# Kernel tuning notes

Measured on AMD Instinct MI355X. Metric: run time of the kernel, lower is better.

## Reference

```python
import jax, jax.numpy as jnp
import numpy as np
import math

HIDDEN = 1024

def setup_inputs() -> dict:
    key = jax.random.key(0)
    k1, k2, k3, k4, k5 = jax.random.split(key, 5)
    s = 1.0 / math.sqrt(HIDDEN)
    return {
        "x": jax.random.normal(k1, (4, 2048, HIDDEN), dtype=jnp.float32),
        "W_qkv": jax.random.uniform(k2, (HIDDEN, 3 * HIDDEN), jnp.float32, -s, s),
        "b_qkv": jax.random.uniform(k3, (3 * HIDDEN,), jnp.float32, -s, s),
        "W_out": jax.random.uniform(k4, (HIDDEN, HIDDEN), jnp.float32, -s, s),
        "b_out": jax.random.uniform(k5, (HIDDEN,), jnp.float32, -s, s),
    }

def reference(x, W_qkv, b_qkv, W_out, b_out):
    # fused QKV projection: [b, s, 3h]
    qkv = jnp.einsum("bsh,hd->bsd", x, W_qkv) + b_qkv
    q, k, v = jnp.split(qkv, 3, axis=-1)
    scale = 1.0 / math.sqrt(x.shape[-1])
    scores = jnp.einsum("bqh,bkh->bqk", q, k) * scale  # [b, s, s]
    attn = jax.nn.softmax(scores, axis=-1)
    out = jnp.einsum("bqk,bkh->bqh", attn, v)
    return jnp.einsum("bsh,hd->bsd", out, W_out) + b_out
```

## Files before the change

kernel.cpp:

```cpp
#include <hip/hip_runtime.h>
#include <cstdint>
#include <cstddef>


typedef __bf16 bf16;
typedef __bf16 bf16x8 __attribute__((ext_vector_type(8)));
typedef __bf16 bf16x4 __attribute__((ext_vector_type(4)));
typedef float  f32x4  __attribute__((ext_vector_type(4)));

#define UNIT 8192

__device__ __forceinline__ void gload_lds16(const bf16* g, bf16* l) {
  __builtin_amdgcn_global_load_lds(
      (const __attribute__((address_space(1))) unsigned int*)g,
      (__attribute__((address_space(3))) unsigned int*)l, 16, 0, 0);
}

#define GATE(N)  asm volatile("s_waitcnt vmcnt(" #N ")" ::: "memory")
#define LGKM0()  asm volatile("s_waitcnt lgkmcnt(0)" ::: "memory")
#define SBAR()   __builtin_amdgcn_s_barrier()
#define SCHED0() __builtin_amdgcn_sched_barrier(0)

#define BK97 32
#define U97  4096

__device__ __forceinline__ void stage97(const bf16* g0, long ld, bf16* u, int tid) {
  const int wv = tid >> 6;
  #pragma unroll
  for (int j = 0; j < 2; ++j) {
    const int c = j * 256 + tid;
    const int r = c >> 2, s = c & 3;
    const int sg = s ^ ((r >> 1) & 3);
    const int cb = j * 256 + (wv << 6);
    gload_lds16(g0 + (long)r * ld + sg * 8, u + (size_t)cb * 8);
  }
}

__device__ __forceinline__ bf16x8 rd97(const bf16* u, int r, int s) {
  return *(const bf16x8*)(u + (size_t)r * 32 + (size_t)((s ^ ((r >> 1) & 3)) * 8));
}

template <int MODE>
__device__ __forceinline__ void gemm97_body(
    const bf16* __restrict__ A, long sAz, int lda,
    const bf16* __restrict__ B, long sBz, int ldb, int K,
    bf16* __restrict__ p0, long sCz, int ldc,
    bf16* __restrict__ p1, bf16* __restrict__ p2,
    float* __restrict__ fout, long sFz,
    const float* __restrict__ bias, float scale) {
  __shared__ bf16 lds[3][2][U97];
  const int tid = threadIdx.x;
  const int wv = tid >> 6, ln = tid & 63;
  const int wr = wv >> 1, wc = wv & 1;
  const int lr = ln & 15, lh = ln >> 4;
  const int m0 = blockIdx.x * 128, n0 = blockIdx.y * 128;
  const int z = blockIdx.z;
  const bf16* Ag = A + (long)z * sAz + (long)m0 * lda;
  const bf16* Bg = B + (long)z * sBz + (long)n0 * ldb;
  const int NT = K / BK97;

  stage97(Ag,        lda, &lds[0][0][0], tid);
  stage97(Bg,        ldb, &lds[0][1][0], tid);
  stage97(Ag + BK97, lda, &lds[1][0][0], tid);
  stage97(Bg + BK97, ldb, &lds[1][1][0], tid);
  GATE(4);
  SCHED0();
  SBAR();

  f32x4 acc[4][4];
  #pragma unroll
  for (int i = 0; i < 4; ++i)
    #pragma unroll
    for (int j = 0; j < 4; ++j) acc[i][j] = f32x4{0.f, 0.f, 0.f, 0.f};

  int rs = 0, ns = 2;
  for (int t = 0; t < NT; ++t) {
    const bf16* Au = &lds[rs][0][0];
    const bf16* Bu = &lds[rs][1][0];
    const bool pf = (t + 2 < NT);
    bf16x8 aF[4], bF[4];
    #pragma unroll
    for (int i = 0; i < 4; ++i) aF[i] = rd97(Au, wr * 64 + i * 16 + lr, lh);
    #pragma unroll
    for (int j = 0; j < 4; ++j) bF[j] = rd97(Bu, wc * 64 + j * 16 + lr, lh);
    if (pf) {
      stage97(Ag + (long)(t + 2) * BK97, lda, &lds[ns][0][0], tid);
      stage97(Bg + (long)(t + 2) * BK97, ldb, &lds[ns][1][0], tid);
    }
    LGKM0();
    SCHED0();
    __builtin_amdgcn_s_setprio(1);
    #pragma unroll
    for (int i = 0; i < 4; ++i)
      #pragma unroll
      for (int j = 0; j < 4; ++j)
        acc[i][j] = __builtin_amdgcn_mfma_f32_16x16x32_bf16(aF[i], bF[j], acc[i][j], 0, 0, 0);
    __builtin_amdgcn_s_setprio(0);
    if (t + 1 < NT) {
      if (pf) { GATE(4); } else { GATE(0); }
      SCHED0();
      SBAR();
    }
    rs = (rs == 2) ? 0 : rs + 1;
    ns = (ns == 2) ? 0 : ns + 1;
  }

  #pragma unroll
  for (int mf = 0; mf < 4; ++mf) {
    #pragma unroll
    for (int nf = 0; nf < 4; ++nf) {
      #pragma unroll
      for (int rg = 0; rg < 4; ++rg) {
        const int gm = m0 + wr * 64 + mf * 16 + lh * 4 + rg;
        const int gn = n0 + wc * 64 + nf * 16 + lr;
        float v = acc[mf][nf][rg];
        if constexpr (MODE == 0) {
          v += bias[gn];
          if (gn < 1024)       p0[(size_t)gm * 1024 + gn] = (bf16)v;
          else if (gn < 2048)  p1[(size_t)gm * 1024 + (gn - 1024)] = (bf16)v;
          else                 p2[(size_t)gm * 1024 + (gn - 2048)] = (bf16)v;
        } else if constexpr (MODE == 2) {
          p0[(size_t)z * sCz + (size_t)gm * ldc + gn] = (bf16)(v * scale);
        } else {
          fout[(size_t)z * sFz + (size_t)gm * ldc + gn] = v + bias[gn];
        }
      }
    }
  }
}

#define GEMM_ARGS const bf16* A, long sAz, int lda, const bf16* B, long sBz, int ldb, \
                  int K, bf16* p0, long sCz, int ldc, bf16* p1, bf16* p2,             \
                  float* fout, long sFz, const float* bias, float scale
__global__ __launch_bounds__(256, 3) void gemm_qkv(GEMM_ARGS) {
  gemm97_body<0>(A, sAz, lda, B, sBz, ldb, K, p0, sCz, ldc, p1, p2, fout, sFz, bias, scale);
}
__global__ __launch_bounds__(256, 3) void gemm_vwt(GEMM_ARGS) {
  gemm97_body<2>(A, sAz, lda, B, sBz, ldb, K, p0, sCz, ldc, p1, p2, fout, sFz, bias, scale);
}
__global__ __launch_bounds__(256, 3) void gemm_pvw(GEMM_ARGS) {
  gemm97_body<3>(A, sAz, lda, B, sBz, ldb, K, p0, sCz, ldc, p1, p2, fout, sFz, bias, scale);
}

#define THREADS8 512

__device__ __forceinline__ void stage_unit(const bf16* g0, long ld, bf16* ldsu, int tid) {
  const int wv = tid >> 6;
  #pragma unroll
  for (int j = 0; j < 2; ++j) {
    const int c = j * 512 + tid;
    const int r = c >> 3;
    const int sg = (c & 7) ^ (r & 7);
    const int cb = j * 512 + (wv << 6);
    gload_lds16(g0 + (long)r * ld + sg * 8, ldsu + (size_t)cb * 8);
  }
}

__device__ __forceinline__ bf16x8 rd_frag(const bf16* unitb, int r, int s) {
  return *(const bf16x8*)(unitb + (size_t)r * 64 + (size_t)((s ^ (r & 7)) * 8));
}

#define PHASE(DB, MH, NH, RA, RB, STAGE_CODE, GATE_CODE)                         \
  {                                                                              \
    if (RA) {                                                                    \
      _Pragma("unroll") for (int mf = 0; mf < 4; ++mf)                           \
        _Pragma("unroll") for (int ks = 0; ks < 2; ++ks)                         \
          aF[mf][ks] = rd_frag(&lds[DB][MH][0], wsm * 64 + mf * 16 + lr, ks * 4 + lh); \
    }                                                                            \
    if (RB) {                                                                    \
      _Pragma("unroll") for (int nf = 0; nf < 2; ++nf)                           \
        _Pragma("unroll") for (int ks = 0; ks < 2; ++ks)                         \
          bF[NH][nf][ks] = rd_frag(&lds[DB][2 + NH][0], wsn * 32 + nf * 16 + lr, ks * 4 + lh); \
    }                                                                            \
    STAGE_CODE;                                                                  \
    SBAR();                                                                      \
    LGKM0();                                                                     \
    SCHED0();                                                                    \
    __builtin_amdgcn_s_setprio(1);                                               \
    _Pragma("unroll") for (int mf = 0; mf < 4; ++mf)                             \
      _Pragma("unroll") for (int nf = 0; nf < 2; ++nf)                           \
        _Pragma("unroll") for (int ks = 0; ks < 2; ++ks)                         \
          acc[(MH)*4 + mf][(NH)*2 + nf] = __builtin_amdgcn_mfma_f32_16x16x32_bf16( \
              aF[mf][ks], bF[NH][nf][ks], acc[(MH)*4 + mf][(NH)*2 + nf], 0, 0, 0); \
    __builtin_amdgcn_s_setprio(0);                                               \
    GATE_CODE;                                                                   \
    SBAR();                                                                      \
    SCHED0();                                                                    \
  }

__global__ __launch_bounds__(THREADS8, 2) void gemm_sc(
    const bf16* __restrict__ A, long sAz, int lda,
    const bf16* __restrict__ B, long sBz, int ldb, int K,
    bf16* __restrict__ p0, long sCz, float scale) {
  __shared__ bf16 lds[2][4][UNIT];
  const int tid = threadIdx.x;
  const int wv = tid >> 6, ln = tid & 63;
  const int wsm = wv >> 2, wsn = wv & 3;
  const int lr = ln & 15, lh = ln >> 4;

  const int gx = gridDim.x, gy = gridDim.y;
  const int lin = blockIdx.x + gx * (blockIdx.y + gy * blockIdx.z);
  const int nwg = gx * gy * gridDim.z;
  const int swz = (lin & 7) * (nwg >> 3) + (lin >> 3);
  const int by = swz % gy;
  const int t2 = swz / gy;
  const int bx = t2 % gx;
  const int z  = t2 / gx;

  const int m0 = bx * 256, n0 = by * 256;
  const bf16* Ag = A + (long)z * sAz + (long)m0 * lda;
  const bf16* Bg = B + (long)z * sBz + (long)n0 * ldb;
  const int NITER = K / 128;

  stage_unit(Ag,             lda, &lds[0][0][0], tid);
  stage_unit(Bg,             ldb, &lds[0][2][0], tid);
  stage_unit(Ag + 128 * lda, lda, &lds[0][1][0], tid);
  stage_unit(Bg + 128 * ldb, ldb, &lds[0][3][0], tid);
  stage_unit(Ag + 64,        lda, &lds[1][0][0], tid);
  stage_unit(Bg + 64,        ldb, &lds[1][2][0], tid);
  GATE(8);
  SBAR();
  SCHED0();

  f32x4 acc[8][4];
  #pragma unroll
  for (int i = 0; i < 8; ++i)
    #pragma unroll
    for (int j = 0; j < 4; ++j) acc[i][j] = f32x4{0.f, 0.f, 0.f, 0.f};
  bf16x8 aF[4][2], bF[2][2][2];

  for (int it = 0; it < NITER; ++it) {
    const bool nl = (it + 1 < NITER);
    const long ktA = 2L * it + 1, ktB = 2L * it + 2, ktC = 2L * it + 3;
    PHASE(0, 0, 0, 1, 1,
      { stage_unit(Ag + 128 * lda + ktA * 64, lda, &lds[1][1][0], tid); },
      { GATE(6); });
    PHASE(0, 0, 1, 0, 1,
      { stage_unit(Bg + 128 * ldb + ktA * 64, ldb, &lds[1][3][0], tid); },
      { GATE(10); });
    PHASE(0, 1, 0, 1, 0,
      { if (nl) stage_unit(Ag + ktB * 64, lda, &lds[0][0][0], tid); },
      {});
    PHASE(0, 1, 1, 0, 0,
      { if (nl) stage_unit(Bg + ktB * 64, ldb, &lds[0][2][0], tid); },
      { if (nl) { GATE(8); } else { GATE(4); } });
    PHASE(1, 0, 0, 1, 1,
      { if (nl) stage_unit(Ag + 128 * lda + ktB * 64, lda, &lds[0][1][0], tid); },
      { if (nl) { GATE(6); } else { GATE(0); } });
    PHASE(1, 0, 1, 0, 1,
      { if (nl) stage_unit(Bg + 128 * ldb + ktB * 64, ldb, &lds[0][3][0], tid); },
      { GATE(10); });
    PHASE(1, 1, 0, 1, 0,
      { if (nl) stage_unit(Ag + ktC * 64, lda, &lds[1][0][0], tid); },
      {});
    PHASE(1, 1, 1, 0, 0,
      { if (nl) stage_unit(Bg + ktC * 64, ldb, &lds[1][2][0], tid); },
      { GATE(8); });
  }

  #pragma unroll
  for (int mi = 0; mi < 8; ++mi) {
    #pragma unroll
    for (int ni = 0; ni < 4; ++ni) {
      #pragma unroll
      for (int rg = 0; rg < 4; ++rg) {
        const int gm = m0 + (mi >> 2) * 128 + wsm * 64 + (mi & 3) * 16 + lh * 4 + rg;
        const int gn = n0 + (ni >> 1) * 128 + wsn * 32 + (ni & 1) * 16 + lr;
        p0[(size_t)z * sCz + (size_t)gm * 2048 + gn] = (bf16)(acc[mi][ni][rg] * scale);
      }
    }
  }
}

__global__ __launch_bounds__(256) void k_f32_to_bf16(const float* __restrict__ in,
                                                     bf16* __restrict__ out, long n) {
  long i = ((long)blockIdx.x * blockDim.x + threadIdx.x) * 4;
  if (i + 3 < n) {
    float4 v = *(const float4*)(in + i);
    bf16x4 o;
    o[0] = (bf16)v.x; o[1] = (bf16)v.y; o[2] = (bf16)v.z; o[3] = (bf16)v.w;
    *(bf16x4*)(out + i) = o;
  }
}

__global__ __launch_bounds__(256) void k_transpose(const float* __restrict__ in,
                                                   bf16* __restrict__ out, int R, int C) {
  __shared__ float t[32][33];
  int c0 = blockIdx.x * 32, r0 = blockIdx.y * 32;
  int tx = threadIdx.x, ty = threadIdx.y;
  #pragma unroll
  for (int dy = 0; dy < 32; dy += 8)
    t[ty + dy][tx] = in[(size_t)(r0 + ty + dy) * C + c0 + tx];
  __syncthreads();
  #pragma unroll
  for (int dy = 0; dy < 32; dy += 8)
    out[(size_t)(c0 + ty + dy) * R + r0 + tx] = (bf16)t[tx][ty + dy];
}

__global__ __launch_bounds__(256) void k_softmax(bf16* __restrict__ S) {
  const int row = blockIdx.x;
  bf16* p = S + (size_t)row * 2048;
  const int tid = threadIdx.x;
  bf16x8 vin = *(const bf16x8*)(p + tid * 8);
  float x[8];
  float mx = -1e30f;
  #pragma unroll
  for (int i = 0; i < 8; ++i) { x[i] = (float)vin[i]; mx = fmaxf(mx, x[i]); }
  #pragma unroll
  for (int off = 32; off; off >>= 1) mx = fmaxf(mx, __shfl_down(mx, off));
  __shared__ float redm[4];
  if ((tid & 63) == 0) redm[tid >> 6] = mx;
  __syncthreads();
  mx = fmaxf(fmaxf(redm[0], redm[1]), fmaxf(redm[2], redm[3]));
  float s = 0.f;
  #pragma unroll
  for (int i = 0; i < 8; ++i) { x[i] = __expf(x[i] - mx); s += x[i]; }
  #pragma unroll
  for (int off = 32; off; off >>= 1) s += __shfl_down(s, off);
  __shared__ float reds[4];
  if ((tid & 63) == 0) reds[tid >> 6] = s;
  __syncthreads();
  s = reds[0] + reds[1] + reds[2] + reds[3];
  float inv = 1.0f / s;
  bf16x8 vo;
  #pragma unroll
  for (int i = 0; i < 8; ++i) vo[i] = (bf16)(x[i] * inv);
  *(bf16x8*)(p + tid * 8) = vo;
}

extern "C" void kernel_launch(void* const* d_in, const int* in_sizes, int n_in,
                              void* d_out, int out_size, void* d_ws, size_t ws_size,
                              hipStream_t stream) {
  const float* x    = (const float*)d_in[0];
  const float* Wqkv = (const float*)d_in[1];
  const float* bqkv = (const float*)d_in[2];
  const float* Wout = (const float*)d_in[3];
  const float* bout = (const float*)d_in[4];
  float* out = (float*)d_out;

  char* w = (char*)d_ws;
  const size_t MB = 1ull << 20;
  bf16* Xb  = (bf16*)(w);
  bf16* WqT = (bf16*)(w + 16 * MB);
  bf16* WoT = (bf16*)(w + 22 * MB);
  bf16* Qb  = (bf16*)(w + 24 * MB);
  bf16* Kb  = (bf16*)(w + 40 * MB);
  bf16* Vb  = (bf16*)(w + 56 * MB);
  bf16* Sb  = (bf16*)(w + 72 * MB);
  bf16* VWT = (bf16*)(w + 104 * MB);

  k_f32_to_bf16<<<8192, 256, 0, stream>>>(x, Xb, 8388608L);
  dim3 tb(32, 8);
  k_transpose<<<dim3(96, 32), tb, 0, stream>>>(Wqkv, WqT, 1024, 3072);
  k_transpose<<<dim3(32, 32), tb, 0, stream>>>(Wout, WoT, 1024, 1024);

  gemm_qkv<<<dim3(64, 24), 256, 0, stream>>>(
      Xb, 0L, 1024, WqT, 0L, 1024, 1024,
      Qb, 0L, 1024, Kb, Vb, nullptr, 0L, bqkv, 1.0f);

  gemm_vwt<<<dim3(8, 16, 4), 256, 0, stream>>>(
      WoT, 0L, 1024, Vb, 2048L * 1024, 1024, 1024,
      VWT, 1024L * 2048, 2048, nullptr, nullptr, nullptr, 0L, nullptr, 1.0f);

  gemm_sc<<<dim3(8, 8, 4), THREADS8, 0, stream>>>(
      Qb, 2048L * 1024, 1024, Kb, 2048L * 1024, 1024, 1024,
      Sb, 2048L * 2048, 0.03125f);

  k_softmax<<<8192, 256, 0, stream>>>(Sb);

  gemm_pvw<<<dim3(16, 8, 4), 256, 0, stream>>>(
      Sb, 2048L * 2048, 2048, VWT, 1024L * 2048, 2048, 2048,
      nullptr, 0L, 1024, nullptr, nullptr, out, 2048L * 1024, bout, 1.0f);
}
```

Before: 209.9 us.

## Load B fragments directly from global into registers, bypassing LDS staging

The GEMM body no longer stages the B tile through LDS. Each wave loads its own B fragments from global memory straight into registers, double-buffered one k-step ahead, while A keeps its triple-buffered LDS pipeline. The loop is manually unrolled by two to alternate the register buffers. This halves LDS traffic and shared-memory footprint, but the B loads are now uncoalesced row-strided per-lane accesses that are repeated across the two wave rows, and their latency is exposed with only one step of prefetch.

```diff
diff --git a/kernel.cpp b/kernel.cpp
--- a/kernel.cpp
+++ b/kernel.cpp
@@ -9,6 +9,7 @@
 typedef float  f32x4  __attribute__((ext_vector_type(4)));
 
 #define UNIT 8192
+#define U97  4096
 
 __device__ __forceinline__ void gload_lds16(const bf16* g, bf16* l) {
   __builtin_amdgcn_global_load_lds(
@@ -20,9 +21,6 @@
 #define LGKM0()  asm volatile("s_waitcnt lgkmcnt(0)" ::: "memory")
 #define SBAR()   __builtin_amdgcn_s_barrier()
 #define SCHED0() __builtin_amdgcn_sched_barrier(0)
-
-#define BK97 32
-#define U97  4096
 
 __device__ __forceinline__ void stage97(const bf16* g0, long ld, bf16* u, int tid) {
   const int wv = tid >> 6;
@@ -38,6 +36,33 @@
 
 __device__ __forceinline__ bf16x8 rd97(const bf16* u, int r, int s) {
   return *(const bf16x8*)(u + (size_t)r * 32 + (size_t)((s ^ ((r >> 1) & 3)) * 8));
+}
+
+template <bool PF2, bool PF1>
+__device__ __forceinline__ void iter97(
+    int t, int rs, int ns, const bf16* Ag, long lda, const bf16* Bl, long ldb,
+    bf16 (*lds)[U97], bf16x8 (&bcur)[4], bf16x8 (&bnxt)[4],
+    f32x4 (&acc)[4][4], int tid, int wr, int lr, int lh) {
+  bf16x8 aF[4];
+  #pragma unroll
+  for (int i = 0; i < 4; ++i) aF[i] = rd97(&lds[rs][0], wr * 64 + i * 16 + lr, lh);
+  if (PF1) {
+    #pragma unroll
+    for (int nf = 0; nf < 4; ++nf)
+      bnxt[nf] = *(const bf16x8*)(Bl + ((long)(t + 1) << 5) + (long)nf * 16 * ldb);
+  }
+  if (PF2) stage97(Ag + (long)(t + 2) * 32, lda, &lds[ns][0], tid);
+  LGKM0();
+  if (PF2) { GATE(6); } else if (PF1) { GATE(4); } else { GATE(0); }
+  SCHED0();
+  __builtin_amdgcn_s_setprio(1);
+  #pragma unroll
+  for (int i = 0; i < 4; ++i)
+    #pragma unroll
+    for (int j = 0; j < 4; ++j)
+      acc[i][j] = __builtin_amdgcn_mfma_f32_16x16x32_bf16(aF[i], bcur[j], acc[i][j], 0, 0, 0);
+  __builtin_amdgcn_s_setprio(0);
+  SBAR();
 }
 
 template <int MODE>
@@ -48,7 +73,7 @@
     bf16* __restrict__ p1, bf16* __restrict__ p2,
     float* __restrict__ fout, long sFz,
     const float* __restrict__ bias, float scale) {
-  __shared__ bf16 lds[3][2][U97];
+  __shared__ bf16 lds[3][U97];
   const int tid = threadIdx.x;
   const int wv = tid >> 6, ln = tid & 63;
   const int wr = wv >> 1, wc = wv & 1;
@@ -57,13 +82,16 @@
   const int z = blockIdx.z;
   const bf16* Ag = A + (long)z * sAz + (long)m0 * lda;
   const bf16* Bg = B + (long)z * sBz + (long)n0 * ldb;
-  const int NT = K / BK97;
-
-  stage97(Ag,        lda, &lds[0][0][0], tid);
-  stage97(Bg,        ldb, &lds[0][1][0], tid);
-  stage97(Ag + BK97, lda, &lds[1][0][0], tid);
-  stage97(Bg + BK97, ldb, &lds[1][1][0], tid);
-  GATE(4);
+  const bf16* Bl = Bg + (size_t)(wc * 64 + lr) * ldb + lh * 8;
+  const int NT = K / 32;
+
+  stage97(Ag,      lda, &lds[0][0], tid);
+  stage97(Ag + 32, lda, &lds[1][0], tid);
+  bf16x8 bX[4], bY[4];
+  #pragma unroll
+  for (int nf = 0; nf < 4; ++nf)
+    bX[nf] = *(const bf16x8*)(Bl + (long)nf * 16 * ldb);
+  GATE(6);
   SCHED0();
   SBAR();
 
@@ -74,36 +102,16 @@
     for (int j = 0; j < 4; ++j) acc[i][j] = f32x4{0.f, 0.f, 0.f, 0.f};
 
   int rs = 0, ns = 2;
-  for (int t = 0; t < NT; ++t) {
-    const bf16* Au = &lds[rs][0][0];
-    const bf16* Bu = &lds[rs][1][0];
-    const bool pf = (t + 2 < NT);
-    bf16x8 aF[4], bF[4];
-    #pragma unroll
-    for (int i = 0; i < 4; ++i) aF[i] = rd97(Au, wr * 64 + i * 16 + lr, lh);
-    #pragma unroll
-    for (int j = 0; j < 4; ++j) bF[j] = rd97(Bu, wc * 64 + j * 16 + lr, lh);
-    if (pf) {
-      stage97(Ag + (long)(t + 2) * BK97, lda, &lds[ns][0][0], tid);
-      stage97(Bg + (long)(t + 2) * BK97, ldb, &lds[ns][1][0], tid);
-    }
-    LGKM0();
-    SCHED0();
-    __builtin_amdgcn_s_setprio(1);
-    #pragma unroll
-    for (int i = 0; i < 4; ++i)
-      #pragma unroll
-      for (int j = 0; j < 4; ++j)
-        acc[i][j] = __builtin_amdgcn_mfma_f32_16x16x32_bf16(aF[i], bF[j], acc[i][j], 0, 0, 0);
-    __builtin_amdgcn_s_setprio(0);
-    if (t + 1 < NT) {
-      if (pf) { GATE(4); } else { GATE(0); }
-      SCHED0();
-      SBAR();
-    }
-    rs = (rs == 2) ? 0 : rs + 1;
-    ns = (ns == 2) ? 0 : ns + 1;
-  }
+  int t = 0;
+  for (; t + 3 < NT; t += 2) {
+    iter97<true, true>(t, rs, ns, Ag, lda, Bl, ldb, lds, bX, bY, acc, tid, wr, lr, lh);
+    rs = (rs == 2) ? 0 : rs + 1;  ns = (ns == 2) ? 0 : ns + 1;
+    iter97<true, true>(t + 1, rs, ns, Ag, lda, Bl, ldb, lds, bY, bX, acc, tid, wr, lr, lh);
+    rs = (rs == 2) ? 0 : rs + 1;  ns = (ns == 2) ? 0 : ns + 1;
+  }
+  iter97<false, true>(t, rs, ns, Ag, lda, Bl, ldb, lds, bX, bY, acc, tid, wr, lr, lh);
+  rs = (rs == 2) ? 0 : rs + 1;  ns = (ns == 2) ? 0 : ns + 1;
+  iter97<false, false>(t + 1, rs, ns, Ag, lda, Bl, ldb, lds, bY, bX, acc, tid, wr, lr, lh);
 
   #pragma unroll
   for (int mf = 0; mf < 4; ++mf) {
```

After: 296.5 us. 1.41x slower.
